# Kernel tuning notes

Hardware: AMD Instinct MI355X
Metric: run time of the kernel (lower is better)

The kernel has to match this reference:

```python
import jax, jax.numpy as jnp
import numpy as np

K = 512        # num_embeddings
D = 64         # embedding_dim
BETA = 0.25
B, S = 64, 4096


def setup_inputs() -> dict:
    key = jax.random.key(0)
    k1, k2 = jax.random.split(key)
    latents = jax.random.normal(k1, (B, S, D), dtype=jnp.float32)
    # torch init: uniform_(-1/K, 1/K)
    embedding = jax.random.uniform(k2, (K, D), dtype=jnp.float32,
                                   minval=-1.0 / K, maxval=1.0 / K)
    return {"latents": latents, "embedding": embedding}


def reference(latents, embedding):
    d = embedding.shape[1]
    flat = latents.reshape(-1, d)                       # [N, D]
    # squared-euclidean distances via norm expansion: [N, K]
    dist = (jnp.sum(flat * flat, axis=1, keepdims=True)
            + jnp.sum(embedding * embedding, axis=1)
            - 2.0 * flat @ embedding.T)
    inds = jnp.argmin(dist, axis=1)                     # [N] (channel = identity)
    # one-hot @ codebook == gather; same math, no [N,K] one-hot materialized
    quantized = embedding[inds].reshape(latents.shape)  # [B, S, D]
    commitment_loss = jnp.mean((jax.lax.stop_gradient(quantized) - latents) ** 2)
    embedding_loss = jnp.mean((quantized - jax.lax.stop_gradient(latents)) ** 2)
    vq_loss = commitment_loss * BETA + embedding_loss
    # straight-through estimator
    quantized_st = latents + jax.lax.stop_gradient(quantized - latents)
    return quantized_st, vq_loss
```

## Files before the change

### kernel.cpp

```cpp
#include <hip/hip_runtime.h>
#include <math.h>
#include <stdint.h>

#define KCODES 512
#define DIM 64
#define NROWS (64 * 4096)
#define BM 512
#define BLOCK 1024
#define NBLK (NROWS / BM)

typedef __bf16 bf16x8 __attribute__((ext_vector_type(8)));
typedef float f32x4 __attribute__((ext_vector_type(4)));

typedef __attribute__((address_space(3))) uint32_t* lds_ptr_t;
typedef const __attribute__((address_space(1))) uint32_t* glb_ptr_t;

__global__ void vq_prep_kernel(const float* __restrict__ emb,
                               float* __restrict__ en1,
                               __bf16* __restrict__ ebf) {
    int k = blockIdx.x * blockDim.x + threadIdx.x;
    if (k >= KCODES) return;
    const float4* e4 = reinterpret_cast<const float4*>(emb + k * DIM);
    float s0 = 0.f, s1 = 0.f, s2 = 0.f, s3 = 0.f;
#pragma unroll
    for (int j = 0; j < 8; ++j) {
        float4 v0 = e4[j * 2];
        float4 v1 = e4[j * 2 + 1];
        s0 = fmaf(v0.x, v0.x, s0); s1 = fmaf(v0.y, v0.y, s1);
        s2 = fmaf(v0.z, v0.z, s2); s3 = fmaf(v0.w, v0.w, s3);
        s0 = fmaf(v1.x, v1.x, s0); s1 = fmaf(v1.y, v1.y, s1);
        s2 = fmaf(v1.z, v1.z, s2); s3 = fmaf(v1.w, v1.w, s3);
        bf16x8 p;
        p[0] = (__bf16)(-2.f * v0.x); p[1] = (__bf16)(-2.f * v0.y);
        p[2] = (__bf16)(-2.f * v0.z); p[3] = (__bf16)(-2.f * v0.w);
        p[4] = (__bf16)(-2.f * v1.x); p[5] = (__bf16)(-2.f * v1.y);
        p[6] = (__bf16)(-2.f * v1.z); p[7] = (__bf16)(-2.f * v1.w);
        *reinterpret_cast<bf16x8*>(&ebf[k * DIM + (j ^ (k & 7)) * 8]) = p;
    }
    en1[k] = 1.0f + (s0 + s1) + (s2 + s3);
}

__launch_bounds__(BLOCK, 8)
__global__ void vq_mfma_kernel(const float* __restrict__ lat,
                               const float* __restrict__ emb,
                               const float* __restrict__ en1,
                               const __bf16* __restrict__ ebf,
                               float* __restrict__ outq,
                               float* __restrict__ partials) {
    __shared__ __align__(16) __bf16 e_lds[KCODES * DIM];
    __shared__ float en_lds[KCODES];
    __shared__ float wsum_lds[BLOCK / 64];

    const int t = threadIdx.x;
    const int lane = t & 63, wid = t >> 6;
    const int l15 = lane & 15, lq = lane >> 4;
    const int swz = l15 & 7;
    const size_t blockrow = (size_t)blockIdx.x * BM;
    const size_t waverow = blockrow + (size_t)wid * 32;

#pragma unroll
    for (int i = 0; i < 4; ++i) {
        int c = t + i * BLOCK;
        __builtin_amdgcn_global_load_lds(
            (glb_ptr_t)(const void*)(ebf + c * 8),
            (lds_ptr_t)(void*)(&e_lds[c * 8]), 16, 0, 0);
    }

    bf16x8 afrag[2][2];
#pragma unroll
    for (int mf = 0; mf < 2; ++mf) {
#pragma unroll
        for (int ks = 0; ks < 2; ++ks) {
            const float* xp =
                lat + (waverow + mf * 16 + l15) * DIM + ks * 32 + lq * 8;
            float4 v0 = reinterpret_cast<const float4*>(xp)[0];
            float4 v1 = reinterpret_cast<const float4*>(xp)[1];
            bf16x8 a;
            a[0] = (__bf16)v0.x; a[1] = (__bf16)v0.y;
            a[2] = (__bf16)v0.z; a[3] = (__bf16)v0.w;
            a[4] = (__bf16)v1.x; a[5] = (__bf16)v1.y;
            a[6] = (__bf16)v1.z; a[7] = (__bf16)v1.w;
            afrag[mf][ks] = a;
        }
    }
    if (t < KCODES) en_lds[t] = en1[t];
    __syncthreads();

    uint32_t best[2][4];
#pragma unroll
    for (int mf = 0; mf < 2; ++mf)
#pragma unroll
        for (int r = 0; r < 4; ++r) best[mf][r] = 0xFFFFFFFFu;

#pragma unroll 4
    for (int nf = 0; nf < 32; ++nf) {
        const int n = nf * 16 + l15;
        bf16x8 b0 = *reinterpret_cast<const bf16x8*>(
            &e_lds[n * DIM + (lq ^ swz) * 8]);
        bf16x8 b1 = *reinterpret_cast<const bf16x8*>(
            &e_lds[n * DIM + ((lq + 4) ^ swz) * 8]);
        float en = en_lds[n];
        f32x4 acc0 = {en, en, en, en};
        f32x4 acc1 = {en, en, en, en};
        acc0 = __builtin_amdgcn_mfma_f32_16x16x32_bf16(afrag[0][0], b0, acc0, 0, 0, 0);
        acc0 = __builtin_amdgcn_mfma_f32_16x16x32_bf16(afrag[0][1], b1, acc0, 0, 0, 0);
        acc1 = __builtin_amdgcn_mfma_f32_16x16x32_bf16(afrag[1][0], b0, acc1, 0, 0, 0);
        acc1 = __builtin_amdgcn_mfma_f32_16x16x32_bf16(afrag[1][1], b1, acc1, 0, 0, 0);
        const uint32_t nn = (uint32_t)n;
#pragma unroll
        for (int r = 0; r < 4; ++r) {
            uint32_t k0 = (__float_as_uint(acc0[r]) & 0xFFFFFE00u) | nn;
            uint32_t k1 = (__float_as_uint(acc1[r]) & 0xFFFFFE00u) | nn;
            best[0][r] = min(best[0][r], k0);
            best[1][r] = min(best[1][r], k1);
        }
    }

#pragma unroll
    for (int off = 1; off < 16; off <<= 1) {
#pragma unroll
        for (int mf = 0; mf < 2; ++mf)
#pragma unroll
            for (int r = 0; r < 4; ++r) {
                uint32_t o = (uint32_t)__shfl_xor((int)best[mf][r], off, 64);
                best[mf][r] = min(best[mf][r], o);
            }
    }

    float lsum = 0.f;
    const float4* emb4 = reinterpret_cast<const float4*>(emb);
    const float4* lat4 = reinterpret_cast<const float4*>(lat);
    float4* out4 = reinterpret_cast<float4*>(outq);
#pragma unroll
    for (int mf = 0; mf < 2; ++mf) {
#pragma unroll
        for (int r = 0; r < 4; ++r) {
            const uint32_t k = best[mf][r] & 511u;
            const size_t grow = waverow + mf * 16 + lq * 4 + r;
            float4 e4 = emb4[k * 16 + l15];
            float4 x4 = lat4[grow * 16 + l15];
            out4[grow * 16 + l15] = e4;
            float d0 = e4.x - x4.x, d1 = e4.y - x4.y;
            float d2 = e4.z - x4.z, d3 = e4.w - x4.w;
            lsum = fmaf(d0, d0, lsum);
            lsum = fmaf(d1, d1, lsum);
            lsum = fmaf(d2, d2, lsum);
            lsum = fmaf(d3, d3, lsum);
        }
    }

#pragma unroll
    for (int off = 32; off > 0; off >>= 1)
        lsum += __shfl_down(lsum, off, 64);
    if (lane == 0) wsum_lds[wid] = lsum;
    __syncthreads();
    if (t == 0) {
        float s = 0.f;
#pragma unroll
        for (int w = 0; w < BLOCK / 64; ++w) s += wsum_lds[w];
        partials[blockIdx.x] = s;
    }
}

__global__ void vq_loss_kernel(const float* __restrict__ partials,
                               float* __restrict__ loss) {
    float s = 0.f;
    for (int i = threadIdx.x; i < NBLK; i += 256) s += partials[i];
#pragma unroll
    for (int off = 32; off > 0; off >>= 1)
        s += __shfl_down(s, off, 64);
    __shared__ float wsum[4];
    const int lane = threadIdx.x & 63;
    const int wid = threadIdx.x >> 6;
    if (lane == 0) wsum[wid] = s;
    __syncthreads();
    if (threadIdx.x == 0) {
        float tsum = 0.f;
#pragma unroll
        for (int w = 0; w < 4; ++w) tsum += wsum[w];
        loss[0] = 1.25f * (tsum / (float)((size_t)NROWS * DIM));
    }
}

extern "C" void kernel_launch(void* const* d_in, const int* in_sizes, int n_in,
                              void* d_out, int out_size, void* d_ws, size_t ws_size,
                              hipStream_t stream) {
    const float* lat = (const float*)d_in[0];
    const float* emb = (const float*)d_in[1];
    float* outq = (float*)d_out;
    float* loss = (float*)d_out + (size_t)NROWS * DIM;

    float* en1 = (float*)d_ws;
    __bf16* ebf = (__bf16*)((char*)d_ws + 2048);
    float* partials = (float*)((char*)d_ws + 67584);

    vq_prep_kernel<<<2, 256, 0, stream>>>(emb, en1, ebf);
    vq_mfma_kernel<<<NBLK, BLOCK, 0, stream>>>(lat, emb, en1, ebf, outq, partials);
    vq_loss_kernel<<<1, 256, 0, stream>>>(partials, loss);
}
```

Measured before the change: 44.83 us.

## Read codebook fragments directly from global memory instead of staging in LDS

Removes the 64KB LDS staging of the bf16 codebook and norms, along with the block-wide barrier. Each wave now loads its B fragments and norms straight from global memory, relying on L1/L2 caching. The block shrinks from 1024 to 256 threads (128 rows per block) and the prep kernel drops the XOR swizzle. This removes LDS occupancy limits and the startup sync, but every wave now repeatedly issues global loads for the whole codebook inside the hot loop, adding cache traffic and latency.

```diff
diff --git a/kernel.cpp b/kernel.cpp
--- a/kernel.cpp
+++ b/kernel.cpp
@@ -5,15 +5,13 @@
 #define KCODES 512
 #define DIM 64
 #define NROWS (64 * 4096)
-#define BM 512
-#define BLOCK 1024
+#define BLOCK 256
+#define ROWS_PER_WAVE 32
+#define BM (BLOCK / 64 * ROWS_PER_WAVE)
 #define NBLK (NROWS / BM)
 
 typedef __bf16 bf16x8 __attribute__((ext_vector_type(8)));
 typedef float f32x4 __attribute__((ext_vector_type(4)));
-
-typedef __attribute__((address_space(3))) uint32_t* lds_ptr_t;
-typedef const __attribute__((address_space(1))) uint32_t* glb_ptr_t;
 
 __global__ void vq_prep_kernel(const float* __restrict__ emb,
                                float* __restrict__ en1,
@@ -35,36 +33,24 @@
         p[2] = (__bf16)(-2.f * v0.z); p[3] = (__bf16)(-2.f * v0.w);
         p[4] = (__bf16)(-2.f * v1.x); p[5] = (__bf16)(-2.f * v1.y);
         p[6] = (__bf16)(-2.f * v1.z); p[7] = (__bf16)(-2.f * v1.w);
-        *reinterpret_cast<bf16x8*>(&ebf[k * DIM + (j ^ (k & 7)) * 8]) = p;
+        *reinterpret_cast<bf16x8*>(&ebf[k * DIM + j * 8]) = p;
     }
     en1[k] = 1.0f + (s0 + s1) + (s2 + s3);
 }
 
-__launch_bounds__(BLOCK, 8)
+__launch_bounds__(BLOCK, 6)
 __global__ void vq_mfma_kernel(const float* __restrict__ lat,
                                const float* __restrict__ emb,
                                const float* __restrict__ en1,
                                const __bf16* __restrict__ ebf,
                                float* __restrict__ outq,
                                float* __restrict__ partials) {
-    __shared__ __align__(16) __bf16 e_lds[KCODES * DIM];
-    __shared__ float en_lds[KCODES];
     __shared__ float wsum_lds[BLOCK / 64];
 
     const int t = threadIdx.x;
     const int lane = t & 63, wid = t >> 6;
     const int l15 = lane & 15, lq = lane >> 4;
-    const int swz = l15 & 7;
-    const size_t blockrow = (size_t)blockIdx.x * BM;
-    const size_t waverow = blockrow + (size_t)wid * 32;
-
-#pragma unroll
-    for (int i = 0; i < 4; ++i) {
-        int c = t + i * BLOCK;
-        __builtin_amdgcn_global_load_lds(
-            (glb_ptr_t)(const void*)(ebf + c * 8),
-            (lds_ptr_t)(void*)(&e_lds[c * 8]), 16, 0, 0);
-    }
+    const size_t waverow = (size_t)blockIdx.x * BM + (size_t)wid * ROWS_PER_WAVE;
 
     bf16x8 afrag[2][2];
 #pragma unroll
@@ -83,8 +69,6 @@
             afrag[mf][ks] = a;
         }
     }
-    if (t < KCODES) en_lds[t] = en1[t];
-    __syncthreads();
 
     uint32_t best[2][4];
 #pragma unroll
@@ -95,11 +79,10 @@
 #pragma unroll 4
     for (int nf = 0; nf < 32; ++nf) {
         const int n = nf * 16 + l15;
-        bf16x8 b0 = *reinterpret_cast<const bf16x8*>(
-            &e_lds[n * DIM + (lq ^ swz) * 8]);
-        bf16x8 b1 = *reinterpret_cast<const bf16x8*>(
-            &e_lds[n * DIM + ((lq + 4) ^ swz) * 8]);
-        float en = en_lds[n];
+        const __bf16* bp = ebf + n * DIM + lq * 8;
+        bf16x8 b0 = *reinterpret_cast<const bf16x8*>(bp);
+        bf16x8 b1 = *reinterpret_cast<const bf16x8*>(bp + 32);
+        float en = en1[n];
         f32x4 acc0 = {en, en, en, en};
         f32x4 acc1 = {en, en, en, en};
         acc0 = __builtin_amdgcn_mfma_f32_16x16x32_bf16(afrag[0][0], b0, acc0, 0, 0, 0);
```

Result: slower. 123.0 us (+174.3%).

## Process two row groups per wave with prefetch and algebraic loss from argmin scores

Applied to the files above, without the earlier changes.

Halves the block size so each wave handles 64 rows in two groups of 32. The second group's latents are prefetched while the first is scored, so each block loads the codebook into LDS once for twice as many rows. The loss is no longer computed by re-reading latents after the gather. It is derived from the winning distance key (masked score minus the 1.0 bias) plus a running sum of x squared, which removes a second global read of the latents. The trade-off is that the loss now comes from the bf16 MFMA distance with its low mantissa bits truncated, a slight precision change.

```diff
diff --git a/kernel.cpp b/kernel.cpp
--- a/kernel.cpp
+++ b/kernel.cpp
@@ -5,8 +5,10 @@
 #define KCODES 512
 #define DIM 64
 #define NROWS (64 * 4096)
-#define BM 512
-#define BLOCK 1024
+#define BLOCK 512
+#define GROUP_ROWS 32
+#define ROWS_PER_WAVE 64
+#define BM ((BLOCK / 64) * ROWS_PER_WAVE)
 #define NBLK (NROWS / BM)
 
 typedef __bf16 bf16x8 __attribute__((ext_vector_type(8)));
@@ -40,7 +42,7 @@
     en1[k] = 1.0f + (s0 + s1) + (s2 + s3);
 }
 
-__launch_bounds__(BLOCK, 8)
+__launch_bounds__(BLOCK, 4)
 __global__ void vq_mfma_kernel(const float* __restrict__ lat,
                                const float* __restrict__ emb,
                                const float* __restrict__ en1,
@@ -55,99 +57,129 @@
     const int lane = t & 63, wid = t >> 6;
     const int l15 = lane & 15, lq = lane >> 4;
     const int swz = l15 & 7;
-    const size_t blockrow = (size_t)blockIdx.x * BM;
-    const size_t waverow = blockrow + (size_t)wid * 32;
-
-#pragma unroll
-    for (int i = 0; i < 4; ++i) {
+    const uint32_t waverow = (uint32_t)blockIdx.x * BM + (uint32_t)wid * ROWS_PER_WAVE;
+
+#pragma unroll
+    for (int i = 0; i < 8; ++i) {
         int c = t + i * BLOCK;
         __builtin_amdgcn_global_load_lds(
             (glb_ptr_t)(const void*)(ebf + c * 8),
             (lds_ptr_t)(void*)(&e_lds[c * 8]), 16, 0, 0);
     }
 
+    float4 araw[2][2][2];
+    auto load_a = [&](int g) {
+#pragma unroll
+        for (int mf = 0; mf < 2; ++mf)
+#pragma unroll
+            for (int ks = 0; ks < 2; ++ks) {
+                const float* xp = lat +
+                    (waverow + (uint32_t)g * GROUP_ROWS + mf * 16 + l15) * DIM +
+                    ks * 32 + lq * 8;
+                araw[mf][ks][0] = reinterpret_cast<const float4*>(xp)[0];
+                araw[mf][ks][1] = reinterpret_cast<const float4*>(xp)[1];
+            }
+    };
+
+    load_a(0);
+    en_lds[t] = en1[t];
+    __syncthreads();
+
+    float xsq = 0.f, lsum = 0.f;
     bf16x8 afrag[2][2];
-#pragma unroll
-    for (int mf = 0; mf < 2; ++mf) {
-#pragma unroll
-        for (int ks = 0; ks < 2; ++ks) {
-            const float* xp =
-                lat + (waverow + mf * 16 + l15) * DIM + ks * 32 + lq * 8;
-            float4 v0 = reinterpret_cast<const float4*>(xp)[0];
-            float4 v1 = reinterpret_cast<const float4*>(xp)[1];
-            bf16x8 a;
-            a[0] = (__bf16)v0.x; a[1] = (__bf16)v0.y;
-            a[2] = (__bf16)v0.z; a[3] = (__bf16)v0.w;
-            a[4] = (__bf16)v1.x; a[5] = (__bf16)v1.y;
-            a[6] = (__bf16)v1.z; a[7] = (__bf16)v1.w;
-            afrag[mf][ks] = a;
-        }
-    }
-    if (t < KCODES) en_lds[t] = en1[t];
-    __syncthreads();
-
     uint32_t best[2][4];
-#pragma unroll
-    for (int mf = 0; mf < 2; ++mf)
-#pragma unroll
-        for (int r = 0; r < 4; ++r) best[mf][r] = 0xFFFFFFFFu;
-
+
+    auto cvt_a = [&]() {
+#pragma unroll
+        for (int mf = 0; mf < 2; ++mf)
+#pragma unroll
+            for (int ks = 0; ks < 2; ++ks) {
+                float4 v0 = araw[mf][ks][0], v1 = araw[mf][ks][1];
+                xsq = fmaf(v0.x, v0.x, xsq); xsq = fmaf(v0.y, v0.y, xsq);
+                xsq = fmaf(v0.z, v0.z, xsq); xsq = fmaf(v0.w, v0.w, xsq);
+                xsq = fmaf(v1.x, v1.x, xsq); xsq = fmaf(v1.y, v1.y, xsq);
+                xsq = fmaf(v1.z, v1.z, xsq); xsq = fmaf(v1.w, v1.w, xsq);
+                bf16x8 a;
+                a[0] = (__bf16)v0.x; a[1] = (__bf16)v0.y;
+                a[2] = (__bf16)v0.z; a[3] = (__bf16)v0.w;
+                a[4] = (__bf16)v1.x; a[5] = (__bf16)v1.y;
+                a[6] = (__bf16)v1.z; a[7] = (__bf16)v1.w;
+                afrag[mf][ks] = a;
+            }
+    };
+
+    auto score = [&]() {
+#pragma unroll
+        for (int mf = 0; mf < 2; ++mf)
+#pragma unroll
+            for (int r = 0; r < 4; ++r) best[mf][r] = 0xFFFFFFFFu;
 #pragma unroll 4
-    for (int nf = 0; nf < 32; ++nf) {
-        const int n = nf * 16 + l15;
-        bf16x8 b0 = *reinterpret_cast<const bf16x8*>(
-            &e_lds[n * DIM + (lq ^ swz) * 8]);
-        bf16x8 b1 = *reinterpret_cast<const bf16x8*>(
-            &e_lds[n * DIM + ((lq + 4) ^ swz) * 8]);
-        float en = en_lds[n];
-        f32x4 acc0 = {en, en, en, en};
-        f32x4 acc1 = {en, en, en, en};
-        acc0 = __builtin_amdgcn_mfma_f32_16x16x32_bf16(afrag[0][0], b0, acc0, 0, 0, 0);
-        acc0 = __builtin_amdgcn_mfma_f32_16x16x32_bf16(afrag[0][1], b1, acc0, 0, 0, 0);
-        acc1 = __builtin_amdgcn_mfma_f32_16x16x32_bf16(afrag[1][0], b0, acc1, 0, 0, 0);
-        acc1 = __builtin_amdgcn_mfma_f32_16x16x32_bf16(afrag[1][1], b1, acc1, 0, 0, 0);
-        const uint32_t nn = (uint32_t)n;
-#pragma unroll
-        for (int r = 0; r < 4; ++r) {
-            uint32_t k0 = (__float_as_uint(acc0[r]) & 0xFFFFFE00u) | nn;
-            uint32_t k1 = (__float_as_uint(acc1[r]) & 0xFFFFFE00u) | nn;
-            best[0][r] = min(best[0][r], k0);
-            best[1][r] = min(best[1][r], k1);
-        }
-    }
-
-#pragma unroll
-    for (int off = 1; off < 16; off <<= 1) {
-#pragma unroll
-        for (int mf = 0; mf < 2; ++mf)
+        for (int nf = 0; nf < 32; ++nf) {
+            const int n = nf * 16 + l15;
+            bf16x8 b0 = *reinterpret_cast<const bf16x8*>(
+                &e_lds[n * DIM + (lq ^ swz) * 8]);
+            bf16x8 b1 = *reinterpret_cast<const bf16x8*>(
+                &e_lds[n * DIM + ((lq + 4) ^ swz) * 8]);
+            float en = en_lds[n];
+            f32x4 acc0 = {en, en, en, en};
+            f32x4 acc1 = {en, en, en, en};
+            acc0 = __builtin_amdgcn_mfma_f32_16x16x32_bf16(afrag[0][0], b0, acc0, 0, 0, 0);
+            acc0 = __builtin_amdgcn_mfma_f32_16x16x32_bf16(afrag[0][1], b1, acc0, 0, 0, 0);
+            acc1 = __builtin_amdgcn_mfma_f32_16x16x32_bf16(afrag[1][0], b0, acc1, 0, 0, 0);
+            acc1 = __builtin_amdgcn_mfma_f32_16x16x32_bf16(afrag[1][1], b1, acc1, 0, 0, 0);
+            const uint32_t nn = (uint32_t)n;
 #pragma unroll
             for (int r = 0; r < 4; ++r) {
-                uint32_t o = (uint32_t)__shfl_xor((int)best[mf][r], off, 64);
-                best[mf][r] = min(best[mf][r], o);
-            }
-    }
-
-    float lsum = 0.f;
-    const float4* emb4 = reinterpret_cast<const float4*>(emb);
-    const float4* lat4 = reinterpret_cast<const float4*>(lat);
-    float4* out4 = reinterpret_cast<float4*>(outq);
-#pragma unroll
-    for (int mf = 0; mf < 2; ++mf) {
-#pragma unroll
-        for (int r = 0; r < 4; ++r) {
-            const uint32_t k = best[mf][r] & 511u;
-            const size_t grow = waverow + mf * 16 + lq * 4 + r;
-            float4 e4 = emb4[k * 16 + l15];
-            float4 x4 = lat4[grow * 16 + l15];
-            out4[grow * 16 + l15] = e4;
-            float d0 = e4.x - x4.x, d1 = e4.y - x4.y;
-            float d2 = e4.z - x4.z, d3 = e4.w - x4.w;
-            lsum = fmaf(d0, d0, lsum);
-            lsum = fmaf(d1, d1, lsum);
-            lsum = fmaf(d2, d2, lsum);
-            lsum = fmaf(d3, d3, lsum);
-        }
-    }
+                uint32_t k0 = (__float_as_uint(acc0[r]) & 0xFFFFFE00u) | nn;
+                uint32_t k1 = (__float_as_uint(acc1[r]) & 0xFFFFFE00u) | nn;
+                best[0][r] = min(best[0][r], k0);
+                best[1][r] = min(best[1][r], k1);
+            }
+        }
+    };
+
+    auto finish = [&](int g) {
+#pragma unroll
+        for (int off = 1; off < 16; off <<= 1) {
+#pragma unroll
+            for (int mf = 0; mf < 2; ++mf)
+#pragma unroll
+                for (int r = 0; r < 4; ++r) {
+                    uint32_t o = (uint32_t)__shfl_xor((int)best[mf][r], off, 64);
+                    best[mf][r] = min(best[mf][r], o);
+                }
+        }
+        if (l15 == 0) {
+#pragma unroll
+            for (int mf = 0; mf < 2; ++mf)
+#pragma unroll
+                for (int r = 0; r < 4; ++r)
+                    lsum += __uint_as_float(best[mf][r] & 0xFFFFFE00u) - 1.0f;
+        }
+        const float4* emb4 = reinterpret_cast<const float4*>(emb);
+        float4* out4 = reinterpret_cast<float4*>(outq);
+#pragma unroll
+        for (int mf = 0; mf < 2; ++mf) {
+#pragma unroll
+            for (int r = 0; r < 4; ++r) {
+                const uint32_t k = best[mf][r] & 511u;
+                const uint32_t grow =
+                    waverow + (uint32_t)g * GROUP_ROWS + mf * 16 + lq * 4 + r;
+                float4 e4 = emb4[k * 16 + l15];
+                out4[grow * 16 + l15] = e4;
+            }
+        }
+    };
+
+    cvt_a();
+    load_a(1);
+    score();
+    finish(0);
+    cvt_a();
+    score();
+    finish(1);
+
+    lsum += xsq;
 
 #pragma unroll
     for (int off = 32; off > 0; off >>= 1)
```

New measurement: 40.90 us. 1.1x faster.
